# Kernel tuning notes

Measured on AMD Instinct MI355X. Metric: run time of the kernel, lower is better.

Reference implementation:

```python
import jax, jax.numpy as jnp
import numpy as np

B, T, EMB, HID, NCLS = 256, 512, 128, 256, 32000


def _forward(X, C_table, U_i, V_i, b_i, U_f, V_f, b_f, U_c, V_c, b_c, U_o, V_o, b_o,
             U_i1, V_i1, b_i1, U_f1, V_f1, b_f1, U_c1, V_c1, b_c1, U_o1, V_o1, b_o1,
             W_w, b_out):
    E = C_table[X]  # [B, T, EMB]
    # Layer 0: in the source, h_t0 and c_t0 are NEVER reassigned inside the loop,
    # so they remain zeros for every timestep. Hence h_t0 @ V_* == 0 and
    # f_t * c_t0 == 0, and layer 0 is time-independent -> vectorize over T.
    i0 = jax.nn.sigmoid(jnp.einsum('bte,eh->bth', E, U_i) + b_i)
    g0 = jnp.tanh(jnp.einsum('bte,eh->bth', E, U_c) + b_c)
    o0 = jax.nn.sigmoid(jnp.einsum('bte,eh->bth', E, U_o) + b_o)
    c0 = i0 * g0               # f_t * c_t0 term is exactly zero
    h0 = o0 * jnp.tanh(c0)     # [B, T, HID]

    # Layer 1: true recurrence over its own (h_t1, c_t1) state, fed by layer-0 h.
    # Computed for faithfulness; the source's output ignores it (results holds h_t).
    def step(carry, x):
        h1, c1 = carry
        i1 = jax.nn.sigmoid(x @ U_i1 + h1 @ V_i1 + b_i1)
        g1 = jnp.tanh(x @ U_c1 + h1 @ V_c1 + b_c1)
        f1 = jax.nn.sigmoid(x @ U_f1 + h1 @ V_f1 + b_f1)
        o1 = jax.nn.sigmoid(x @ U_o1 + h1 @ V_o1 + b_o1)
        c1n = f1 * c1 + i1 * g1
        h1n = o1 * jnp.tanh(c1n)
        return (h1n, c1n), None

    zeros = jnp.zeros((h0.shape[0], HID), dtype=h0.dtype)
    _carry, _ = jax.lax.scan(step, (zeros, zeros), jnp.swapaxes(h0, 0, 1))

    # outputs = results[-1] = layer-0 hidden at the last timestep
    logits = h0[:, -1, :] @ W_w.T + b_out  # [B, NCLS]
    return logits


def setup_inputs() -> dict:
    key = jax.random.key(0)
    ks = jax.random.split(key, 32)

    def p(k, *shape):
        return (jax.random.normal(k, shape, dtype=jnp.float32) * 0.02)

    inp = {
        'X': jax.random.randint(ks[0], (B, T), 0, NCLS, dtype=jnp.int32),
        'C_table': p(ks[1], NCLS, EMB),
        'U_i': p(ks[2], EMB, HID), 'V_i': p(ks[3], HID, HID), 'b_i': p(ks[4], HID),
        'U_f': p(ks[5], EMB, HID), 'V_f': p(ks[6], HID, HID), 'b_f': p(ks[7], HID),
        'U_c': p(ks[8], EMB, HID), 'V_c': p(ks[9], HID, HID), 'b_c': p(ks[10], HID),
        'U_o': p(ks[11], EMB, HID), 'V_o': p(ks[12], HID, HID), 'b_o': p(ks[13], HID),
        'U_i1': p(ks[14], HID, HID), 'V_i1': p(ks[15], HID, HID), 'b_i1': p(ks[16], HID),
        'U_f1': p(ks[17], HID, HID), 'V_f1': p(ks[18], HID, HID), 'b_f1': p(ks[19], HID),
        'U_c1': p(ks[20], HID, HID), 'V_c1': p(ks[21], HID, HID), 'b_c1': p(ks[22], HID),
        'U_o1': p(ks[23], HID, HID), 'V_o1': p(ks[24], HID, HID), 'b_o1': p(ks[25], HID),
        'W_w': p(ks[26], NCLS, HID),
        'b_out': jnp.ones((NCLS,), dtype=jnp.float32),
    }
    return inp


def reference(X, C_table, U_i, V_i, b_i, U_f, V_f, b_f, U_c, V_c, b_c, U_o, V_o, b_o,
              U_i1, V_i1, b_i1, U_f1, V_f1, b_f1, U_c1, V_c1, b_c1, U_o1, V_o1, b_o1,
              W_w, b_out):
    return _forward(X, C_table, U_i, V_i, b_i, U_f, V_f, b_f, U_c, V_c, b_c,
                    U_o, V_o, b_o, U_i1, V_i1, b_i1, U_f1, V_f1, b_f1,
                    U_c1, V_c1, b_c1, U_o1, V_o1, b_o1, W_w, b_out)
```

## Files before the change

### kernel.cpp

```cpp
#include <hip/hip_runtime.h>

#define B_SZ   256
#define T_SZ   512
#define EMB    128
#define HID    256
#define NCLS   32000

typedef __attribute__((ext_vector_type(8))) short short8;
typedef __attribute__((ext_vector_type(4))) float f32x4;

__device__ inline unsigned short bf16rne(float f) {
    union { float f; unsigned int u; } v; v.f = f;
    unsigned int u = v.u;
    u += 0x7FFFu + ((u >> 16) & 1u);
    return (unsigned short)(u >> 16);
}
__device__ inline unsigned pkhi(float lo, float hi) {
    union { float f; unsigned u; } a, b;
    a.f = lo; b.f = hi;
    return ((b.u + 0x8000u) & 0xFFFF0000u) | ((a.u + 0x8000u) >> 16);
}


__global__ __launch_bounds__(512, 2)
void lstm_h_last(const int* __restrict__ X, const float* __restrict__ C_table,
                 const float* __restrict__ U_i, const float* __restrict__ b_i,
                 const float* __restrict__ U_c, const float* __restrict__ b_c,
                 const float* __restrict__ U_o, const float* __restrict__ b_o,
                 unsigned short* __restrict__ hws) {
    __shared__ float e[2][EMB];
    __shared__ int   tok[2];
    __shared__ f32x4 part[8][3][2][64];

    const int t    = threadIdx.x;
    const int wid  = t >> 6;
    const int lane = t & 63;
    const int m0   = blockIdx.x * 2;
    const int kb   = lane * 4;

    if (t < 2) tok[t] = X[(size_t)(m0 + t) * T_SZ + (T_SZ - 1)];
    __syncthreads();
    if (t < 256) e[t >> 7][t & 127] =
        C_table[(size_t)tok[t >> 7] * EMB + (t & 127)];
    __syncthreads();

    f32x4 acc[3][2] = {};
    #pragma unroll 4
    for (int j = 0; j < 16; ++j) {
        const int ee = wid * 16 + j;
        const f32x4 ui = *reinterpret_cast<const f32x4*>(U_i + (size_t)ee * HID + kb);
        const f32x4 uc = *reinterpret_cast<const f32x4*>(U_c + (size_t)ee * HID + kb);
        const f32x4 uo = *reinterpret_cast<const f32x4*>(U_o + (size_t)ee * HID + kb);
        #pragma unroll
        for (int r = 0; r < 2; ++r) {
            const float ev = e[r][ee];
            acc[0][r] += ev * ui;
            acc[1][r] += ev * uc;
            acc[2][r] += ev * uo;
        }
    }
    #pragma unroll
    for (int g = 0; g < 3; ++g)
        #pragma unroll
        for (int r = 0; r < 2; ++r)
            part[wid][g][r][lane] = acc[g][r];
    __syncthreads();

    if (t < 128) {
        const int r = wid;
        const int m = m0 + r;
        f32x4 s[3];
        #pragma unroll
        for (int g = 0; g < 3; ++g) {
            s[g] = part[0][g][r][lane];
            #pragma unroll
            for (int w = 1; w < 8; ++w) s[g] += part[w][g][r][lane];
        }
        const f32x4 bi = *reinterpret_cast<const f32x4*>(b_i + kb);
        const f32x4 bc = *reinterpret_cast<const f32x4*>(b_c + kb);
        const f32x4 bo = *reinterpret_cast<const f32x4*>(b_o + kb);
        float h[4];
        #pragma unroll
        for (int c = 0; c < 4; ++c) {
            const float i0 = 1.f / (1.f + expf(-(s[0][c] + bi[c])));
            const float g0 = tanhf(s[1][c] + bc[c]);
            const float o0 = 1.f / (1.f + expf(-(s[2][c] + bo[c])));
            h[c] = o0 * tanhf(i0 * g0);
        }
        const int frag = (m >> 4) * 8 + (lane >> 3);
        const int li   = ((lane >> 1) & 3) * 16 + (m & 15);
        unsigned* dst = reinterpret_cast<unsigned*>(
            hws + frag * 512 + li * 8 + (lane & 1) * 4);
        dst[0] = pkhi(h[0], h[1]);
        dst[1] = pkhi(h[2], h[3]);
    }
}

__global__ __launch_bounds__(512, 2)
void logits_gemm(const unsigned short* __restrict__ hws,
                 const float* __restrict__ Ww,
                 const float* __restrict__ b_out,
                 float* __restrict__ out) {
    __shared__ unsigned short Hs[B_SZ * HID];

    const int t    = threadIdx.x;
    const int wid  = t >> 6;
    const int lane = t & 63;
    const int l15  = lane & 15;
    const int lq   = lane >> 4;

    const int nbase = blockIdx.x * 128 + wid * 16;

    const float* wrow = Ww + (size_t)(nbase + l15) * HID + lq * 8;
    f32x4 wf[16];
    #pragma unroll
    for (int ks = 0; ks < 8; ++ks) {
        wf[2 * ks]     = *reinterpret_cast<const f32x4*>(wrow + ks * 32);
        wf[2 * ks + 1] = *reinterpret_cast<const f32x4*>(wrow + ks * 32 + 4);
    }

    #pragma unroll
    for (int j = 0; j < 16; ++j) {
        const unsigned short* src = hws + (wid * 16 + j) * 512;
        __builtin_amdgcn_global_load_lds(
            (const __attribute__((address_space(1))) unsigned int*)(src + lane * 8),
            (__attribute__((address_space(3))) unsigned int*)(Hs + (wid * 16 + j) * 512),
            16, 0, 0);
    }

    #pragma unroll
    for (int i = 0; i < 16; ++i) asm volatile("" : "+v"(wf[i]));
    asm volatile("s_waitcnt vmcnt(0)" ::: "memory");
    __builtin_amdgcn_s_barrier();
    __builtin_amdgcn_sched_barrier(0);

    short8 aw[8];
    #pragma unroll
    for (int ks = 0; ks < 8; ++ks) {
        union { short8 s; unsigned u[4]; } p;
        p.u[0] = pkhi(wf[2 * ks][0],     wf[2 * ks][1]);
        p.u[1] = pkhi(wf[2 * ks][2],     wf[2 * ks][3]);
        p.u[2] = pkhi(wf[2 * ks + 1][0], wf[2 * ks + 1][1]);
        p.u[3] = pkhi(wf[2 * ks + 1][2], wf[2 * ks + 1][3]);
        aw[ks] = p.s;
    }

    f32x4 bv = *reinterpret_cast<const f32x4*>(b_out + nbase + lq * 4);

    const unsigned short* hbase = Hs + lane * 8;
    f32x4 acc[16] = {};
    #pragma unroll
    for (int ks = 0; ks < 8; ++ks) {
        #pragma unroll
        for (int mf = 0; mf < 16; ++mf) {
            short8 bh = *reinterpret_cast<const short8*>(
                hbase + (mf * 8 + ks) * 512);
            acc[mf] = __builtin_amdgcn_mfma_f32_16x16x32_bf16(
                aw[ks], bh, acc[mf], 0, 0, 0);
        }
    }

    #pragma unroll
    for (int mf = 0; mf < 16; ++mf) {
        f32x4 o = acc[mf] + bv;
        *reinterpret_cast<f32x4*>(
            out + (size_t)(mf * 16 + l15) * NCLS + nbase + lq * 4) = o;
    }
}

extern "C" void kernel_launch(void* const* d_in, const int* in_sizes, int n_in,
                              void* d_out, int out_size, void* d_ws, size_t ws_size,
                              hipStream_t stream) {
    const int*   X       = (const int*)  d_in[0];
    const float* C_table = (const float*)d_in[1];
    const float* U_i     = (const float*)d_in[2];
    const float* b_i     = (const float*)d_in[4];
    const float* U_c     = (const float*)d_in[8];
    const float* b_c     = (const float*)d_in[10];
    const float* U_o     = (const float*)d_in[11];
    const float* b_o     = (const float*)d_in[13];
    const float* W_w     = (const float*)d_in[26];
    const float* b_out   = (const float*)d_in[27];
    float* out = (float*)d_out;

    unsigned short* hws = (unsigned short*)d_ws;

    lstm_h_last<<<B_SZ / 2, 512, 0, stream>>>(X, C_table, U_i, b_i, U_c, b_c,
                                              U_o, b_o, hws);
    logits_gemm<<<NCLS / 128, 512, 0, stream>>>(hws, W_w, b_out, out);
}
```

Baseline: 28.54 us.

## Process two N-tiles per block, overlapping second W load with first tile's MFMA

Result: slower. 37.24 us (+30.5%).

```diff
diff --git a/kernel.cpp b/kernel.cpp
--- a/kernel.cpp
+++ b/kernel.cpp
@@ -109,15 +109,11 @@
     const int l15  = lane & 15;
     const int lq   = lane >> 4;
 
-    const int nbase = blockIdx.x * 128 + wid * 16;
-
-    const float* wrow = Ww + (size_t)(nbase + l15) * HID + lq * 8;
-    f32x4 wf[16];
-    #pragma unroll
-    for (int ks = 0; ks < 8; ++ks) {
-        wf[2 * ks]     = *reinterpret_cast<const f32x4*>(wrow + ks * 32);
-        wf[2 * ks + 1] = *reinterpret_cast<const f32x4*>(wrow + ks * 32 + 4);
-    }
+    const int nb0 = blockIdx.x * 256 + wid * 16;
+    const int nb1 = nb0 + 128;
+
+    f32x4 bv0 = *reinterpret_cast<const f32x4*>(b_out + nb0 + lq * 4);
+    f32x4 bv1 = *reinterpret_cast<const f32x4*>(b_out + nb1 + lq * 4);
 
     #pragma unroll
     for (int j = 0; j < 16; ++j) {
@@ -128,9 +124,26 @@
             16, 0, 0);
     }
 
-    #pragma unroll
-    for (int i = 0; i < 16; ++i) asm volatile("" : "+v"(wf[i]));
-    asm volatile("s_waitcnt vmcnt(0)" ::: "memory");
+    const float* wrow0 = Ww + (size_t)(nb0 + l15) * HID + lq * 8;
+    const float* wrow1 = Ww + (size_t)(nb1 + l15) * HID + lq * 8;
+    f32x4 wf0[16], wf1[16];
+    #pragma unroll
+    for (int ks = 0; ks < 8; ++ks) {
+        wf0[2 * ks]     = *reinterpret_cast<const f32x4*>(wrow0 + ks * 32);
+        wf0[2 * ks + 1] = *reinterpret_cast<const f32x4*>(wrow0 + ks * 32 + 4);
+    }
+    #pragma unroll
+    for (int ks = 0; ks < 8; ++ks) {
+        wf1[2 * ks]     = *reinterpret_cast<const f32x4*>(wrow1 + ks * 32);
+        wf1[2 * ks + 1] = *reinterpret_cast<const f32x4*>(wrow1 + ks * 32 + 4);
+    }
+
+    asm volatile("" : "+v"(bv0), "+v"(bv1));
+    #pragma unroll
+    for (int i = 0; i < 16; ++i) asm volatile("" : "+v"(wf0[i]), "+v"(wf1[i]));
+    __builtin_amdgcn_sched_barrier(0);
+
+    asm volatile("s_waitcnt vmcnt(16)" ::: "memory");
     __builtin_amdgcn_s_barrier();
     __builtin_amdgcn_sched_barrier(0);
 
@@ -138,33 +151,62 @@
     #pragma unroll
     for (int ks = 0; ks < 8; ++ks) {
         union { short8 s; unsigned u[4]; } p;
-        p.u[0] = pkhi(wf[2 * ks][0],     wf[2 * ks][1]);
-        p.u[1] = pkhi(wf[2 * ks][2],     wf[2 * ks][3]);
-        p.u[2] = pkhi(wf[2 * ks + 1][0], wf[2 * ks + 1][1]);
-        p.u[3] = pkhi(wf[2 * ks + 1][2], wf[2 * ks + 1][3]);
+        p.u[0] = pkhi(wf0[2 * ks][0],     wf0[2 * ks][1]);
+        p.u[1] = pkhi(wf0[2 * ks][2],     wf0[2 * ks][3]);
+        p.u[2] = pkhi(wf0[2 * ks + 1][0], wf0[2 * ks + 1][1]);
+        p.u[3] = pkhi(wf0[2 * ks + 1][2], wf0[2 * ks + 1][3]);
         aw[ks] = p.s;
     }
-
-    f32x4 bv = *reinterpret_cast<const f32x4*>(b_out + nbase + lq * 4);
-
     const unsigned short* hbase = Hs + lane * 8;
-    f32x4 acc[16] = {};
-    #pragma unroll
-    for (int ks = 0; ks < 8; ++ks) {
+    {
+        f32x4 acc[16] = {};
+        #pragma unroll
+        for (int ks = 0; ks < 8; ++ks)
+            #pragma unroll
+            for (int mf = 0; mf < 16; ++mf) {
+                short8 bh = *reinterpret_cast<const short8*>(
+                    hbase + (mf * 8 + ks) * 512);
+                acc[mf] = __builtin_amdgcn_mfma_f32_16x16x32_bf16(
+                    aw[ks], bh, acc[mf], 0, 0, 0);
+            }
         #pragma unroll
         for (int mf = 0; mf < 16; ++mf) {
-            short8 bh = *reinterpret_cast<const short8*>(
-                hbase + (mf * 8 + ks) * 512);
-            acc[mf] = __builtin_amdgcn_mfma_f32_16x16x32_bf16(
-                aw[ks], bh, acc[mf], 0, 0, 0);
-        }
-    }
-
-    #pragma unroll
-    for (int mf = 0; mf < 16; ++mf) {
-        f32x4 o = acc[mf] + bv;
-        *reinterpret_cast<f32x4*>(
-            out + (size_t)(mf * 16 + l15) * NCLS + nbase + lq * 4) = o;
+            f32x4 o = acc[mf] + bv0;
+            *reinterpret_cast<f32x4*>(
+                out + (size_t)(mf * 16 + l15) * NCLS + nb0 + lq * 4) = o;
+        }
+    }
+    __builtin_amdgcn_sched_barrier(0);
+
+    asm volatile("s_waitcnt vmcnt(16)" ::: "memory");
+    __builtin_amdgcn_sched_barrier(0);
+
+    #pragma unroll
+    for (int ks = 0; ks < 8; ++ks) {
+        union { short8 s; unsigned u[4]; } p;
+        p.u[0] = pkhi(wf1[2 * ks][0],     wf1[2 * ks][1]);
+        p.u[1] = pkhi(wf1[2 * ks][2],     wf1[2 * ks][3]);
+        p.u[2] = pkhi(wf1[2 * ks + 1][0], wf1[2 * ks + 1][1]);
+        p.u[3] = pkhi(wf1[2 * ks + 1][2], wf1[2 * ks + 1][3]);
+        aw[ks] = p.s;
+    }
+    {
+        f32x4 acc[16] = {};
+        #pragma unroll
+        for (int ks = 0; ks < 8; ++ks)
+            #pragma unroll
+            for (int mf = 0; mf < 16; ++mf) {
+                short8 bh = *reinterpret_cast<const short8*>(
+                    hbase + (mf * 8 + ks) * 512);
+                acc[mf] = __builtin_amdgcn_mfma_f32_16x16x32_bf16(
+                    aw[ks], bh, acc[mf], 0, 0, 0);
+            }
+        #pragma unroll
+        for (int mf = 0; mf < 16; ++mf) {
+            f32x4 o = acc[mf] + bv1;
+            *reinterpret_cast<f32x4*>(
+                out + (size_t)(mf * 16 + l15) * NCLS + nb1 + lq * 4) = o;
+        }
     }
 }
 
@@ -187,5 +229,5 @@
 
     lstm_h_last<<<B_SZ / 2, 512, 0, stream>>>(X, C_table, U_i, b_i, U_c, b_c,
                                               U_o, b_o, hws);
-    logits_gemm<<<NCLS / 128, 512, 0, stream>>>(hws, W_w, b_out, out);
-}
+    logits_gemm<<<NCLS / 256, 512, 0, stream>>>(hws, W_w, b_out, out);
+}
```

## Restructure logits GEMM to stage W in LDS and keep H in registers

Applied to the files above, without the earlier changes.

Result: slower. 31.25 us (+9.5%).

```diff
diff --git a/kernel.cpp b/kernel.cpp
--- a/kernel.cpp
+++ b/kernel.cpp
@@ -101,7 +101,7 @@
                  const float* __restrict__ Ww,
                  const float* __restrict__ b_out,
                  float* __restrict__ out) {
-    __shared__ unsigned short Hs[B_SZ * HID];
+    __shared__ float Wlds[64 * HID];
 
     const int t    = threadIdx.x;
     const int wid  = t >> 6;
@@ -109,62 +109,71 @@
     const int l15  = lane & 15;
     const int lq   = lane >> 4;
 
-    const int nbase = blockIdx.x * 128 + wid * 16;
-
-    const float* wrow = Ww + (size_t)(nbase + l15) * HID + lq * 8;
-    f32x4 wf[16];
-    #pragma unroll
-    for (int ks = 0; ks < 8; ++ks) {
-        wf[2 * ks]     = *reinterpret_cast<const f32x4*>(wrow + ks * 32);
-        wf[2 * ks + 1] = *reinterpret_cast<const f32x4*>(wrow + ks * 32 + 4);
-    }
-
-    #pragma unroll
-    for (int j = 0; j < 16; ++j) {
-        const unsigned short* src = hws + (wid * 16 + j) * 512;
+    const int n0 = blockIdx.x * 64;
+    const int mw = wid * 32;
+
+    short8 bh[16];
+    #pragma unroll
+    for (int mf = 0; mf < 2; ++mf)
+        #pragma unroll
+        for (int ks = 0; ks < 8; ++ks) {
+            const int f = ((mw >> 4) + mf) * 8 + ks;
+            bh[mf * 8 + ks] = *reinterpret_cast<const short8*>(
+                hws + f * 512 + lane * 8);
+        }
+
+    #pragma unroll
+    for (int i = 0; i < 8; ++i) {
+        const int r = wid * 8 + i;
+        const float* src = Ww + (size_t)(n0 + r) * HID + ((lane ^ (r & 7)) << 2);
         __builtin_amdgcn_global_load_lds(
-            (const __attribute__((address_space(1))) unsigned int*)(src + lane * 8),
-            (__attribute__((address_space(3))) unsigned int*)(Hs + (wid * 16 + j) * 512),
+            (const __attribute__((address_space(1))) unsigned int*)src,
+            (__attribute__((address_space(3))) unsigned int*)(Wlds + r * HID),
             16, 0, 0);
     }
 
     #pragma unroll
-    for (int i = 0; i < 16; ++i) asm volatile("" : "+v"(wf[i]));
+    for (int i = 0; i < 16; ++i) asm volatile("" : "+v"(bh[i]));
     asm volatile("s_waitcnt vmcnt(0)" ::: "memory");
     __builtin_amdgcn_s_barrier();
     __builtin_amdgcn_sched_barrier(0);
 
-    short8 aw[8];
-    #pragma unroll
-    for (int ks = 0; ks < 8; ++ks) {
-        union { short8 s; unsigned u[4]; } p;
-        p.u[0] = pkhi(wf[2 * ks][0],     wf[2 * ks][1]);
-        p.u[1] = pkhi(wf[2 * ks][2],     wf[2 * ks][3]);
-        p.u[2] = pkhi(wf[2 * ks + 1][0], wf[2 * ks + 1][1]);
-        p.u[3] = pkhi(wf[2 * ks + 1][2], wf[2 * ks + 1][3]);
-        aw[ks] = p.s;
-    }
-
-    f32x4 bv = *reinterpret_cast<const f32x4*>(b_out + nbase + lq * 4);
-
-    const unsigned short* hbase = Hs + lane * 8;
-    f32x4 acc[16] = {};
-    #pragma unroll
-    for (int ks = 0; ks < 8; ++ks) {
-        #pragma unroll
-        for (int mf = 0; mf < 16; ++mf) {
-            short8 bh = *reinterpret_cast<const short8*>(
-                hbase + (mf * 8 + ks) * 512);
-            acc[mf] = __builtin_amdgcn_mfma_f32_16x16x32_bf16(
-                aw[ks], bh, acc[mf], 0, 0, 0);
-        }
-    }
-
-    #pragma unroll
-    for (int mf = 0; mf < 16; ++mf) {
-        f32x4 o = acc[mf] + bv;
-        *reinterpret_cast<f32x4*>(
-            out + (size_t)(mf * 16 + l15) * NCLS + nbase + lq * 4) = o;
+    #pragma unroll
+    for (int s = 0; s < 4; ++s) {
+        f32x4 bv = *reinterpret_cast<const f32x4*>(b_out + n0 + s * 16 + lq * 4);
+
+        const int R  = s * 16 + l15;
+        const int sw = R & 7;
+        const float* rp = Wlds + R * HID;
+        short8 aw[8];
+        #pragma unroll
+        for (int ks = 0; ks < 8; ++ks) {
+            const int j0 = ks * 8 + lq * 2;
+            f32x4 a0 = *reinterpret_cast<const f32x4*>(rp + ((j0 ^ sw) << 2));
+            f32x4 a1 = *reinterpret_cast<const f32x4*>(rp + (((j0 + 1) ^ sw) << 2));
+            union { short8 v; unsigned u[4]; } p;
+            p.u[0] = pkhi(a0[0], a0[1]);
+            p.u[1] = pkhi(a0[2], a0[3]);
+            p.u[2] = pkhi(a1[0], a1[1]);
+            p.u[3] = pkhi(a1[2], a1[3]);
+            aw[ks] = p.v;
+        }
+
+        f32x4 acc[2] = {};
+        #pragma unroll
+        for (int ks = 0; ks < 8; ++ks)
+            #pragma unroll
+            for (int mf = 0; mf < 2; ++mf)
+                acc[mf] = __builtin_amdgcn_mfma_f32_16x16x32_bf16(
+                    aw[ks], bh[mf * 8 + ks], acc[mf], 0, 0, 0);
+
+        #pragma unroll
+        for (int mf = 0; mf < 2; ++mf) {
+            const int m = mw + mf * 16 + l15;
+            f32x4 o = acc[mf] + bv;
+            *reinterpret_cast<f32x4*>(
+                out + (size_t)m * NCLS + n0 + s * 16 + lq * 4) = o;
+        }
     }
 }
 
@@ -187,5 +196,5 @@
 
     lstm_h_last<<<B_SZ / 2, 512, 0, stream>>>(X, C_table, U_i, b_i, U_c, b_c,
                                               U_o, b_o, hws);
-    logits_gemm<<<NCLS / 128, 512, 0, stream>>>(hws, W_w, b_out, out);
-}
+    logits_gemm<<<NCLS / 64, 512, 0, stream>>>(hws, W_w, b_out, out);
+}
```
